# Kernel tuning notes

Hardware: AMD Instinct MI355X
Metric: run time of the kernel (lower is better)

The kernel has to match this reference:

```python
import jax, jax.numpy as jnp
import numpy as np

NUM_HEADS = 16
HEAD_DIM = 128
RMS_EPS = 1e-6


def _rms_norm(x):
    # RMSNorm over last dim, no learned weight
    return x * jax.lax.rsqrt(jnp.mean(jnp.square(x), axis=-1, keepdims=True) + RMS_EPS)


def _rotary_cos_sin(T, head_dim, dtype=jnp.float32):
    # half-truncated RoPE: quarter of dims get frequencies, next quarter gets freq 0
    dim_quarter = max(1, head_dim // 4)
    angular_freq = (1.0 / 1024.0) ** jnp.linspace(0.0, 1.0, dim_quarter, dtype=dtype)
    angular_freq = jnp.concatenate([angular_freq, jnp.zeros(dim_quarter, dtype=dtype)])  # [head_dim//2]
    t = jnp.arange(T, dtype=dtype)
    theta = t[:, None] * angular_freq[None, :]  # [T, head_dim//2]
    return jnp.cos(theta), jnp.sin(theta)


def _apply_rotary(x_BTHD, cos, sin):
    # x: [B,T,H,D]; cos/sin: [T, D//2]
    c = cos[None, :, None, :]
    s = sin[None, :, None, :]
    x1, x2 = jnp.split(x_BTHD, 2, axis=-1)
    y1 = x1 * c + x2 * s
    y2 = -x1 * s + x2 * c
    return jnp.concatenate([y1, y2], axis=-1)


def setup_inputs() -> dict:
    key = jax.random.key(0)
    k1, k2, k3 = jax.random.split(key, 3)
    B, T, dim = 1, 2048, 2048
    hdim = NUM_HEADS * HEAD_DIM
    std = 0.5 * dim ** (-0.5)
    x = jax.random.normal(k1, (B, T, dim), dtype=jnp.float32)
    Wqkv = jax.random.normal(k2, (3, hdim, dim), dtype=jnp.float32) * std
    Wout = jax.random.normal(k3, (dim, hdim), dtype=jnp.float32) * std
    return {"x": x, "Wqkv": Wqkv, "Wout": Wout}


def reference(x, Wqkv, Wout):
    B, T, dim = x.shape
    H, D = NUM_HEADS, HEAD_DIM
    scale = 1.0 / (D ** 0.5)

    # fused QKV projection: [B,T,3,H,D]
    qkv = jnp.einsum('btd,ehd->bteh'.replace('eh', 'f'), x, Wqkv.reshape(3 * H * D, dim))  # [B,T,3HD]
    qkv = qkv.reshape(B, T, 3, H, D)
    q, k, v = qkv[:, :, 0], qkv[:, :, 1], qkv[:, :, 2]  # each [B,T,H,D]

    q, k = _rms_norm(q), _rms_norm(k)
    cos, sin = _rotary_cos_sin(T, D, dtype=jnp.float32)
    q, k = _apply_rotary(q, cos, sin), _apply_rotary(k, cos, sin)

    # causal attention
    scores = jnp.einsum('bthd,bshd->bhts', q, k) * scale  # [B,H,T,T]
    causal = jnp.tril(jnp.ones((T, T), dtype=bool))
    scores = jnp.where(causal[None, None], scores, -jnp.inf)
    probs = jax.nn.softmax(scores, axis=-1)
    y = jnp.einsum('bhts,bshd->bthd', probs, v)  # [B,T,H,D]

    y = y.reshape(B, T, H * D)
    return y @ Wout.T
```

## Files before the change

kernel.cpp:

```cpp
#include <hip/hip_runtime.h>
#include <hip/hip_bf16.h>
#include <stdint.h>

typedef __hip_bfloat16 bf16;
typedef __bf16 bf16x8 __attribute__((ext_vector_type(8)));
typedef float f32x4 __attribute__((ext_vector_type(4)));

#define MFMA16(a, b, c) __builtin_amdgcn_mfma_f32_16x16x32_bf16((a), (b), (c), 0, 0, 0)

__device__ __forceinline__ void gload_lds16(const void* g, void* l) {
    __builtin_amdgcn_global_load_lds((const __attribute__((address_space(1))) void*)g,
                                     (__attribute__((address_space(3))) void*)l, 16, 0, 0);
}

struct alignas(16) B8 { bf16 v[8]; };

__global__ __launch_bounds__(256) void cast_all_k(
    const float* __restrict__ x, const float* __restrict__ wqkv, const float* __restrict__ wout,
    bf16* __restrict__ xb, bf16* __restrict__ wqkvb, bf16* __restrict__ woutb) {
    const size_t NX = (size_t)2048 * 2048 / 8;
    const size_t NW = (size_t)3 * 2048 * 2048 / 8;
    size_t i = (size_t)blockIdx.x * 256 + threadIdx.x;
    const float* s; bf16* d;
    if (i < NX)            { s = x;    d = xb; }
    else if (i < NX + NW)  { s = wqkv; d = wqkvb; i -= NX; }
    else                   { s = wout; d = woutb; i -= NX + NW; }
    float4 a = ((const float4*)s)[2 * i];
    float4 b = ((const float4*)s)[2 * i + 1];
    B8 t;
    t.v[0] = __float2bfloat16(a.x); t.v[1] = __float2bfloat16(a.y);
    t.v[2] = __float2bfloat16(a.z); t.v[3] = __float2bfloat16(a.w);
    t.v[4] = __float2bfloat16(b.x); t.v[5] = __float2bfloat16(b.y);
    t.v[6] = __float2bfloat16(b.z); t.v[7] = __float2bfloat16(b.w);
    ((B8*)d)[i] = t;
}

__global__ __launch_bounds__(256) void gemm_bt(
    const bf16* __restrict__ A, const bf16* __restrict__ B, float* __restrict__ C,
    int M, int N, int K) {
    __shared__ __align__(16) bf16 As[128 * 32];
    __shared__ __align__(16) bf16 Bs[128 * 32];
    const int t = threadIdx.x;
    const int lane = t & 63, w = t >> 6;
    const int wr = w >> 1, wc = w & 1;
    const int l15 = lane & 15, lg = lane >> 4;
    const int m0 = blockIdx.y * 128, n0 = blockIdx.x * 128;

    f32x4 acc[4][4] = {};

    for (int k0 = 0; k0 < K; k0 += 32) {
#pragma unroll
        for (int c = 0; c < 2; ++c) {
            int f = t + c * 256;
            int row = f >> 2, cb = f & 3;
            gload_lds16(&A[(size_t)(m0 + row) * K + k0 + cb * 8], &As[f * 8]);
            gload_lds16(&B[(size_t)(n0 + row) * K + k0 + cb * 8], &Bs[f * 8]);
        }
        __syncthreads();

        bf16x8 af[4], bfr[4];
#pragma unroll
        for (int mi = 0; mi < 4; ++mi)
            af[mi] = *(const bf16x8*)&As[(wr * 64 + mi * 16 + l15) * 32 + lg * 8];
#pragma unroll
        for (int ni = 0; ni < 4; ++ni)
            bfr[ni] = *(const bf16x8*)&Bs[(wc * 64 + ni * 16 + l15) * 32 + lg * 8];
#pragma unroll
        for (int mi = 0; mi < 4; ++mi)
#pragma unroll
            for (int ni = 0; ni < 4; ++ni)
                acc[mi][ni] = MFMA16(af[mi], bfr[ni], acc[mi][ni]);
        __syncthreads();
    }

#pragma unroll
    for (int mi = 0; mi < 4; ++mi) {
        int r0 = m0 + wr * 64 + mi * 16 + lg * 4;
#pragma unroll
        for (int ni = 0; ni < 4; ++ni) {
            int c0 = n0 + wc * 64 + ni * 16 + l15;
#pragma unroll
            for (int j = 0; j < 4; ++j)
                C[(size_t)(r0 + j) * N + c0] = acc[mi][ni][j];
        }
    }
}

__global__ __launch_bounds__(128) void normrope_k(
    const float* __restrict__ qkv,
    bf16* __restrict__ qb, bf16* __restrict__ kb, bf16* __restrict__ vb) {
    const int t = blockIdx.x;
    const int h = blockIdx.y;
    const int d = threadIdx.x;
    const float* base = qkv + (size_t)t * 6144;
    float q = base[h * 128 + d];
    float k = base[2048 + h * 128 + d];
    float v = base[4096 + h * 128 + d];

    __shared__ float red[4];
    __shared__ float qn[128], kn[128];
    float sq = q * q, sk = k * k;
#pragma unroll
    for (int m = 1; m <= 32; m <<= 1) {
        sq += __shfl_xor(sq, m);
        sk += __shfl_xor(sk, m);
    }
    if ((d & 63) == 0) { red[(d >> 6) * 2] = sq; red[(d >> 6) * 2 + 1] = sk; }
    __syncthreads();
    float rq = rsqrtf((red[0] + red[2]) * (1.0f / 128.0f) + 1e-6f);
    float rk = rsqrtf((red[1] + red[3]) * (1.0f / 128.0f) + 1e-6f);
    qn[d] = q * rq;
    kn[d] = k * rk;
    __syncthreads();

    int j = d & 63;
    float c = 1.0f, s = 0.0f;
    if (j < 32) {
        float af = exp2f(-10.0f * (float)j / 31.0f);
        float theta = (float)t * af;
        sincosf(theta, &s, &c);
    }
    float oq, ok;
    if (d < 64) { oq =  qn[d] * c + qn[d + 64] * s;  ok =  kn[d] * c + kn[d + 64] * s; }
    else        { oq = -qn[d - 64] * s + qn[d] * c;  ok = -kn[d - 64] * s + kn[d] * c; }

    size_t oidx = ((size_t)h * 2048 + t) * 128 + d;
    qb[oidx] = __float2bfloat16(oq * 0.08838834764831845f);
    kb[oidx] = __float2bfloat16(ok);
    vb[oidx] = __float2bfloat16(v);
}

__global__ __launch_bounds__(256) void attn_k(
    const bf16* __restrict__ qg, const bf16* __restrict__ kg,
    const bf16* __restrict__ vg, bf16* __restrict__ y) {
    const int T = 2048, D = 128;
    const int qt = blockIdx.x, h = blockIdx.y;
    const int qb0 = qt * 64;

    __shared__ __align__(16) bf16 Ks[32 * 128];
    __shared__ __align__(16) bf16 Vt[128 * 40];
    __shared__ __align__(16) bf16 Ps[4][16 * 64];

    const int t = threadIdx.x;
    const int lane = t & 63, w = t >> 6;
    const int l15 = lane & 15, lg = lane >> 4;

    const size_t qoff = ((size_t)h * T + qb0 + w * 16 + l15) * D;
    bf16x8 qf[4];
#pragma unroll
    for (int ks = 0; ks < 4; ++ks)
        qf[ks] = *(const bf16x8*)&qg[qoff + ks * 32 + lg * 8];

    f32x4 o[8] = {};
    float mrow[4] = {-1e30f, -1e30f, -1e30f, -1e30f};
    float lrow[4] = {0.f, 0.f, 0.f, 0.f};

    const int vkey = t & 31, vdc = t >> 5;
    const int ntiles = 2 * qt + 2;

    for (int kt = 0; kt < ntiles; ++kt) {
        const int k0 = kt * 32;
#pragma unroll
        for (int c = 0; c < 2; ++c) {
            int f = t + c * 256;
            int row = f >> 4;
            int cbl = (f ^ row) & 15;
            gload_lds16(&kg[((size_t)h * T + k0 + row) * D + cbl * 8], &Ks[f * 8]);
        }
        {
            const bf16* vsrc = &vg[((size_t)h * T + k0 + vkey) * D + vdc * 16];
            uint4 v0 = *(const uint4*)vsrc;
            uint4 v1 = *(const uint4*)(vsrc + 8);
            const bf16* vv0 = (const bf16*)&v0;
            const bf16* vv1 = (const bf16*)&v1;
#pragma unroll
            for (int i = 0; i < 8; ++i) {
                Vt[(vdc * 16 + i) * 40 + vkey] = vv0[i];
                Vt[(vdc * 16 + 8 + i) * 40 + vkey] = vv1[i];
            }
        }
        __syncthreads();

        f32x4 sc[2] = {};
#pragma unroll
        for (int ks = 0; ks < 4; ++ks) {
#pragma unroll
            for (int nb = 0; nb < 2; ++nb) {
                int row = nb * 16 + l15;
                int cb = ks * 4 + lg;
                bf16x8 kf = *(const bf16x8*)&Ks[row * 128 + ((cb ^ row) & 15) * 8];
                sc[nb] = MFMA16(qf[ks], kf, sc[nb]);
            }
        }

        const int qrow_base = qb0 + w * 16 + lg * 4;
#pragma unroll
        for (int j = 0; j < 4; ++j) {
            float s0 = sc[0][j], s1 = sc[1][j];
            int qrow = qrow_base + j;
            if (k0 + l15 > qrow)      s0 = -1e30f;
            if (k0 + 16 + l15 > qrow) s1 = -1e30f;
            float tm = fmaxf(s0, s1);
            tm = fmaxf(tm, __shfl_xor(tm, 1));
            tm = fmaxf(tm, __shfl_xor(tm, 2));
            tm = fmaxf(tm, __shfl_xor(tm, 4));
            tm = fmaxf(tm, __shfl_xor(tm, 8));
            float mnew = fmaxf(mrow[j], tm);
            float fac = __expf(mrow[j] - mnew);
            float p0 = __expf(s0 - mnew);
            float p1 = __expf(s1 - mnew);
            float ps = p0 + p1;
            ps += __shfl_xor(ps, 1);
            ps += __shfl_xor(ps, 2);
            ps += __shfl_xor(ps, 4);
            ps += __shfl_xor(ps, 8);
            lrow[j] = lrow[j] * fac + ps;
            mrow[j] = mnew;
#pragma unroll
            for (int nd = 0; nd < 8; ++nd) o[nd][j] *= fac;
            int prow = lg * 4 + j;
            int kb0 = l15 >> 3, kb1 = 2 + kb0;
            Ps[w][prow * 64 + ((kb0 ^ (prow & 7)) << 3) + (l15 & 7)] = __float2bfloat16(p0);
            Ps[w][prow * 64 + ((kb1 ^ (prow & 7)) << 3) + (l15 & 7)] = __float2bfloat16(p1);
        }

        bf16x8 pf = *(const bf16x8*)&Ps[w][l15 * 64 + ((lg ^ (l15 & 7)) << 3)];
#pragma unroll
        for (int nd = 0; nd < 8; ++nd) {
            bf16x8 vf = *(const bf16x8*)&Vt[(nd * 16 + l15) * 40 + lg * 8];
            o[nd] = MFMA16(pf, vf, o[nd]);
        }
        __syncthreads();
    }

#pragma unroll
    for (int j = 0; j < 4; ++j) {
        float inv = 1.0f / lrow[j];
        int qrow = qb0 + w * 16 + lg * 4 + j;
#pragma unroll
        for (int nd = 0; nd < 8; ++nd)
            y[(size_t)qrow * 2048 + h * 128 + nd * 16 + l15] =
                __float2bfloat16(o[nd][j] * inv);
    }
}

extern "C" void kernel_launch(void* const* d_in, const int* in_sizes, int n_in,
                              void* d_out, int out_size, void* d_ws, size_t ws_size,
                              hipStream_t stream) {
    const float* x    = (const float*)d_in[0];
    const float* wqkv = (const float*)d_in[1];
    const float* wout = (const float*)d_in[2];
    float* out = (float*)d_out;

    char* ws = (char*)d_ws;
    bf16*  xb    = (bf16*)(ws);
    bf16*  wqkvb = (bf16*)(ws + 8388608);
    bf16*  woutb = (bf16*)(ws + 33554432);
    float* qkvf  = (float*)(ws + 41943040);
    bf16*  qb    = (bf16*)(ws + 92274688);
    bf16*  kb    = (bf16*)(ws + 100663296);
    bf16*  vb    = (bf16*)(ws + 109051904);
    bf16*  yb    = (bf16*)(ws + 117440512);

    cast_all_k<<<10240, 256, 0, stream>>>(x, wqkv, wout, xb, wqkvb, woutb);
    gemm_bt<<<dim3(48, 16), 256, 0, stream>>>(xb, wqkvb, qkvf, 2048, 6144, 2048);
    normrope_k<<<dim3(2048, 16), 128, 0, stream>>>(qkvf, qb, kb, vb);
    attn_k<<<dim3(32, 16), 256, 0, stream>>>(qb, kb, vb, yb);
    gemm_bt<<<dim3(16, 16), 256, 0, stream>>>(yb, woutb, out, 2048, 2048, 2048);
}
```

Before: 388.2 us.

## Split causal attention over key chunks with merge kernel and pre-transposed V

Attention is split into up to four 512-key chunks per query tile (flash-decoding style), and each chunk writes partial max, sum and output to a scratch buffer that reuses the qkv float workspace. A separate merge kernel combines the partials and writes bf16 output. V is pre-transposed into a [H,D,T] bf16 layout by a new kernel so both K and V tiles can be loaded with direct global-to-LDS loads, and the key tile grows from 32 to 64 with causal masking applied only on the diagonal tile. This aims to balance load across the triangular workload and raise occupancy, at the cost of extra partial-result traffic, an extra kernel launch and overwriting qkvf after normrope.

```diff
diff --git a/kernel.cpp b/kernel.cpp
--- a/kernel.cpp
+++ b/kernel.cpp
@@ -14,6 +14,7 @@
 }
 
 struct alignas(16) B8 { bf16 v[8]; };
+struct alignas(8)  B4 { bf16 v[4]; };
 
 __global__ __launch_bounds__(256) void cast_all_k(
     const float* __restrict__ x, const float* __restrict__ wqkv, const float* __restrict__ wout,
@@ -87,15 +88,11 @@
 }
 
 __global__ __launch_bounds__(128) void normrope_k(
-    const float* __restrict__ qkv,
-    bf16* __restrict__ qb, bf16* __restrict__ kb, bf16* __restrict__ vb) {
-    const int t = blockIdx.x;
-    const int h = blockIdx.y;
-    const int d = threadIdx.x;
+    const float* __restrict__ qkv, bf16* __restrict__ qb, bf16* __restrict__ kb) {
+    const int t = blockIdx.x, h = blockIdx.y, d = threadIdx.x;
     const float* base = qkv + (size_t)t * 6144;
     float q = base[h * 128 + d];
     float k = base[2048 + h * 128 + d];
-    float v = base[4096 + h * 128 + d];
 
     __shared__ float red[4];
     __shared__ float qn[128], kn[128];
@@ -127,18 +124,47 @@
     size_t oidx = ((size_t)h * 2048 + t) * 128 + d;
     qb[oidx] = __float2bfloat16(oq * 0.08838834764831845f);
     kb[oidx] = __float2bfloat16(ok);
-    vb[oidx] = __float2bfloat16(v);
-}
-
-__global__ __launch_bounds__(256) void attn_k(
+}
+
+__global__ __launch_bounds__(256) void vtrans_k(
+    const float* __restrict__ qkv, bf16* __restrict__ vt) {
+    __shared__ bf16 Ts[64][72];
+    const int t0 = blockIdx.x * 64, d0 = blockIdx.y * 64, h = blockIdx.z;
+    const int tid = threadIdx.x;
+#pragma unroll
+    for (int it = 0; it < 4; ++it) {
+        int f = tid + it * 256;
+        int tl = f >> 4, dl = (f & 15) * 4;
+        float4 v = *(const float4*)&qkv[(size_t)(t0 + tl) * 6144 + 4096 + h * 128 + d0 + dl];
+        Ts[tl][dl + 0] = __float2bfloat16(v.x);
+        Ts[tl][dl + 1] = __float2bfloat16(v.y);
+        Ts[tl][dl + 2] = __float2bfloat16(v.z);
+        Ts[tl][dl + 3] = __float2bfloat16(v.w);
+    }
+    __syncthreads();
+#pragma unroll
+    for (int it = 0; it < 2; ++it) {
+        int f = tid + it * 256;
+        int dl = f >> 3, tc = f & 7;
+        B8 p;
+#pragma unroll
+        for (int i = 0; i < 8; ++i) p.v[i] = Ts[tc * 8 + i][dl];
+        *(B8*)&vt[((size_t)h * 128 + d0 + dl) * 2048 + t0 + tc * 8] = p;
+    }
+}
+
+__global__ __launch_bounds__(256) void attn_main_k(
     const bf16* __restrict__ qg, const bf16* __restrict__ kg,
-    const bf16* __restrict__ vg, bf16* __restrict__ y) {
+    const bf16* __restrict__ vt, float* __restrict__ part) {
     const int T = 2048, D = 128;
-    const int qt = blockIdx.x, h = blockIdx.y;
+    const int cz = blockIdx.x, qt = blockIdx.y, h = blockIdx.z;
+    if (cz > (qt >> 3)) return;
     const int qb0 = qt * 64;
-
-    __shared__ __align__(16) bf16 Ks[32 * 128];
-    __shared__ __align__(16) bf16 Vt[128 * 40];
+    const int kstart = cz * 512;
+    const int kend = min(kstart + 512, (qt + 1) * 64);
+
+    __shared__ __align__(16) bf16 Ks[64 * 128];
+    __shared__ __align__(16) bf16 Vt[128 * 64];
     __shared__ __align__(16) bf16 Ps[4][16 * 64];
 
     const int t = threadIdx.x;
@@ -155,61 +181,53 @@
     float mrow[4] = {-1e30f, -1e30f, -1e30f, -1e30f};
     float lrow[4] = {0.f, 0.f, 0.f, 0.f};
 
-    const int vkey = t & 31, vdc = t >> 5;
-    const int ntiles = 2 * qt + 2;
-
-    for (int kt = 0; kt < ntiles; ++kt) {
-        const int k0 = kt * 32;
-#pragma unroll
-        for (int c = 0; c < 2; ++c) {
+    for (int k0 = kstart; k0 < kend; k0 += 64) {
+#pragma unroll
+        for (int c = 0; c < 4; ++c) {
             int f = t + c * 256;
-            int row = f >> 4;
-            int cbl = (f ^ row) & 15;
-            gload_lds16(&kg[((size_t)h * T + k0 + row) * D + cbl * 8], &Ks[f * 8]);
-        }
-        {
-            const bf16* vsrc = &vg[((size_t)h * T + k0 + vkey) * D + vdc * 16];
-            uint4 v0 = *(const uint4*)vsrc;
-            uint4 v1 = *(const uint4*)(vsrc + 8);
-            const bf16* vv0 = (const bf16*)&v0;
-            const bf16* vv1 = (const bf16*)&v1;
-#pragma unroll
-            for (int i = 0; i < 8; ++i) {
-                Vt[(vdc * 16 + i) * 40 + vkey] = vv0[i];
-                Vt[(vdc * 16 + 8 + i) * 40 + vkey] = vv1[i];
-            }
+            int krow = f >> 4, kc = f & 15;
+            gload_lds16(&kg[((size_t)h * T + k0 + krow) * D + ((kc ^ (krow & 15)) * 8)],
+                        &Ks[f * 8]);
+            int dr = f >> 3, vc = f & 7;
+            gload_lds16(&vt[((size_t)h * D + dr) * T + k0 + ((vc ^ (dr & 7)) * 8)],
+                        &Vt[f * 8]);
         }
         __syncthreads();
 
-        f32x4 sc[2] = {};
+        f32x4 sc[4] = {};
 #pragma unroll
         for (int ks = 0; ks < 4; ++ks) {
 #pragma unroll
-            for (int nb = 0; nb < 2; ++nb) {
-                int row = nb * 16 + l15;
-                int cb = ks * 4 + lg;
-                bf16x8 kf = *(const bf16x8*)&Ks[row * 128 + ((cb ^ row) & 15) * 8];
+            for (int nb = 0; nb < 4; ++nb) {
+                int key = nb * 16 + l15;
+                int c = ks * 4 + lg;
+                bf16x8 kf = *(const bf16x8*)&Ks[key * 128 + ((c ^ (key & 15)) * 8)];
                 sc[nb] = MFMA16(qf[ks], kf, sc[nb]);
             }
         }
 
+        const bool diag = (k0 == qb0);
         const int qrow_base = qb0 + w * 16 + lg * 4;
 #pragma unroll
         for (int j = 0; j < 4; ++j) {
-            float s0 = sc[0][j], s1 = sc[1][j];
-            int qrow = qrow_base + j;
-            if (k0 + l15 > qrow)      s0 = -1e30f;
-            if (k0 + 16 + l15 > qrow) s1 = -1e30f;
-            float tm = fmaxf(s0, s1);
+            float s0 = sc[0][j], s1 = sc[1][j], s2 = sc[2][j], s3 = sc[3][j];
+            if (diag) {
+                int qrow = qrow_base + j;
+                if (k0 + l15 > qrow)      s0 = -1e30f;
+                if (k0 + 16 + l15 > qrow) s1 = -1e30f;
+                if (k0 + 32 + l15 > qrow) s2 = -1e30f;
+                if (k0 + 48 + l15 > qrow) s3 = -1e30f;
+            }
+            float tm = fmaxf(fmaxf(s0, s1), fmaxf(s2, s3));
             tm = fmaxf(tm, __shfl_xor(tm, 1));
             tm = fmaxf(tm, __shfl_xor(tm, 2));
             tm = fmaxf(tm, __shfl_xor(tm, 4));
             tm = fmaxf(tm, __shfl_xor(tm, 8));
             float mnew = fmaxf(mrow[j], tm);
             float fac = __expf(mrow[j] - mnew);
-            float p0 = __expf(s0 - mnew);
-            float p1 = __expf(s1 - mnew);
-            float ps = p0 + p1;
+            float p0 = __expf(s0 - mnew), p1 = __expf(s1 - mnew);
+            float p2 = __expf(s2 - mnew), p3 = __expf(s3 - mnew);
+            float ps = (p0 + p1) + (p2 + p3);
             ps += __shfl_xor(ps, 1);
             ps += __shfl_xor(ps, 2);
             ps += __shfl_xor(ps, 4);
@@ -219,28 +237,89 @@
 #pragma unroll
             for (int nd = 0; nd < 8; ++nd) o[nd][j] *= fac;
             int prow = lg * 4 + j;
-            int kb0 = l15 >> 3, kb1 = 2 + kb0;
-            Ps[w][prow * 64 + ((kb0 ^ (prow & 7)) << 3) + (l15 & 7)] = __float2bfloat16(p0);
-            Ps[w][prow * 64 + ((kb1 ^ (prow & 7)) << 3) + (l15 & 7)] = __float2bfloat16(p1);
-        }
-
-        bf16x8 pf = *(const bf16x8*)&Ps[w][l15 * 64 + ((lg ^ (l15 & 7)) << 3)];
-#pragma unroll
-        for (int nd = 0; nd < 8; ++nd) {
-            bf16x8 vf = *(const bf16x8*)&Vt[(nd * 16 + l15) * 40 + lg * 8];
-            o[nd] = MFMA16(pf, vf, o[nd]);
+            int sub = l15 & 7, hi = l15 >> 3;
+            bf16* pw = &Ps[w][prow * 64 + sub];
+            pw[(((0 + hi) ^ (prow & 7)) * 8)] = __float2bfloat16(p0);
+            pw[(((2 + hi) ^ (prow & 7)) * 8)] = __float2bfloat16(p1);
+            pw[(((4 + hi) ^ (prow & 7)) * 8)] = __float2bfloat16(p2);
+            pw[(((6 + hi) ^ (prow & 7)) * 8)] = __float2bfloat16(p3);
+        }
+
+#pragma unroll
+        for (int hk = 0; hk < 2; ++hk) {
+            bf16x8 pf = *(const bf16x8*)&Ps[w][l15 * 64 + (((hk * 4 + lg) ^ (l15 & 7)) * 8)];
+#pragma unroll
+            for (int nd = 0; nd < 8; ++nd) {
+                int dd = nd * 16 + l15;
+                bf16x8 vf = *(const bf16x8*)&Vt[dd * 64 + (((hk * 4 + lg) ^ (dd & 7)) * 8)];
+                o[nd] = MFMA16(pf, vf, o[nd]);
+            }
         }
         __syncthreads();
     }
 
-#pragma unroll
-    for (int j = 0; j < 4; ++j) {
-        float inv = 1.0f / lrow[j];
-        int qrow = qb0 + w * 16 + lg * 4 + j;
-#pragma unroll
-        for (int nd = 0; nd < 8; ++nd)
-            y[(size_t)qrow * 2048 + h * 128 + nd * 16 + l15] =
-                __float2bfloat16(o[nd][j] * inv);
+    int b = qt >> 3, rr = qt & 7;
+    int slot = h * 80 + qt + 4 * b * (b - 1) + rr * b + cz;
+    float* rec = part + (size_t)slot * 8320;
+    if (l15 == 0) {
+#pragma unroll
+        for (int j = 0; j < 4; ++j) {
+            rec[w * 16 + lg * 4 + j] = mrow[j];
+            rec[64 + w * 16 + lg * 4 + j] = lrow[j];
+        }
+    }
+#pragma unroll
+    for (int nd = 0; nd < 8; ++nd)
+#pragma unroll
+        for (int j = 0; j < 4; ++j)
+            rec[128 + (w * 16 + lg * 4 + j) * 128 + nd * 16 + l15] = o[nd][j];
+}
+
+__global__ __launch_bounds__(256) void attn_merge_k(
+    const float* __restrict__ part, bf16* __restrict__ y) {
+    const int qt = blockIdx.x, h = blockIdx.y, tid = threadIdx.x;
+    const int nch = (qt >> 3) + 1;
+    int b = qt >> 3, rr = qt & 7;
+    const int base = h * 80 + qt + 4 * b * (b - 1) + rr * b;
+    const int r = tid >> 2;
+    const int d0 = (tid & 3) * 32;
+
+    float mi[4], li[4], wgt[4];
+    float M = -1e30f;
+#pragma unroll
+    for (int i = 0; i < 4; ++i) {
+        if (i < nch) {
+            mi[i] = part[(size_t)(base + i) * 8320 + r];
+            li[i] = part[(size_t)(base + i) * 8320 + 64 + r];
+            M = fmaxf(M, mi[i]);
+        } else { mi[i] = -1e30f; li[i] = 0.f; }
+    }
+    float L = 0.f;
+#pragma unroll
+    for (int i = 0; i < 4; ++i) {
+        wgt[i] = (i < nch) ? __expf(mi[i] - M) : 0.f;
+        L += li[i] * wgt[i];
+    }
+    float invL = 1.0f / L;
+
+    bf16* yrow = &y[(size_t)(qt * 64 + r) * 2048 + h * 128 + d0];
+#pragma unroll
+    for (int dd = 0; dd < 32; dd += 4) {
+        float a0 = 0.f, a1 = 0.f, a2 = 0.f, a3 = 0.f;
+#pragma unroll
+        for (int i = 0; i < 4; ++i) {
+            if (i < nch) {
+                const float4 ov = *(const float4*)&part[(size_t)(base + i) * 8320 + 128 + r * 128 + d0 + dd];
+                a0 += wgt[i] * ov.x; a1 += wgt[i] * ov.y;
+                a2 += wgt[i] * ov.z; a3 += wgt[i] * ov.w;
+            }
+        }
+        B4 p;
+        p.v[0] = __float2bfloat16(a0 * invL);
+        p.v[1] = __float2bfloat16(a1 * invL);
+        p.v[2] = __float2bfloat16(a2 * invL);
+        p.v[3] = __float2bfloat16(a3 * invL);
+        *(B4*)&yrow[dd] = p;
     }
 }
 
@@ -259,12 +338,14 @@
     float* qkvf  = (float*)(ws + 41943040);
     bf16*  qb    = (bf16*)(ws + 92274688);
     bf16*  kb    = (bf16*)(ws + 100663296);
-    bf16*  vb    = (bf16*)(ws + 109051904);
+    bf16*  vt    = (bf16*)(ws + 109051904);
     bf16*  yb    = (bf16*)(ws + 117440512);
 
     cast_all_k<<<10240, 256, 0, stream>>>(x, wqkv, wout, xb, wqkvb, woutb);
     gemm_bt<<<dim3(48, 16), 256, 0, stream>>>(xb, wqkvb, qkvf, 2048, 6144, 2048);
-    normrope_k<<<dim3(2048, 16), 128, 0, stream>>>(qkvf, qb, kb, vb);
-    attn_k<<<dim3(32, 16), 256, 0, stream>>>(qb, kb, vb, yb);
+    normrope_k<<<dim3(2048, 16), 128, 0, stream>>>(qkvf, qb, kb);
+    vtrans_k<<<dim3(32, 2, 16), 256, 0, stream>>>(qkvf, vt);
+    attn_main_k<<<dim3(4, 32, 16), 256, 0, stream>>>(qb, kb, vt, qkvf);
+    attn_merge_k<<<dim3(32, 16), 256, 0, stream>>>(qkvf, yb);
     gemm_bt<<<dim3(16, 16), 256, 0, stream>>>(yb, woutb, out, 2048, 2048, 2048);
 }
```

Result: no change. 388.3 us (+0.0%).
